# Performance work log

Measured on AMD Instinct MI355X. Metric: run time of the kernel, lower is better.

The kernel has to match this reference:

```python
import jax, jax.numpy as jnp
import numpy as np

N = 100000
E = 1600000
NEG_SLOPE = 0.2


def gat_conv(h_x, edge_index, W, a_src, a_dst, b, heads, concat):
    # h_x: [N, Fin]; W: [Fin, heads*C]
    n = h_x.shape[0]
    h = (h_x @ W).reshape(n, heads, -1)              # [N, H, C]
    s_src = (h * a_src[None]).sum(-1)                # [N, H]
    s_dst = (h * a_dst[None]).sum(-1)                # [N, H]
    # add self loops (PyG default)
    loop = jnp.arange(n, dtype=edge_index.dtype)
    src = jnp.concatenate([edge_index[0], loop])
    dst = jnp.concatenate([edge_index[1], loop])
    e = jax.nn.leaky_relu(s_src[src] + s_dst[dst], NEG_SLOPE)   # [E+N, H]
    m = jax.ops.segment_max(e, dst, num_segments=n)
    e = jnp.exp(e - m[dst])
    denom = jax.ops.segment_sum(e, dst, num_segments=n)
    alpha = e / denom[dst]                                       # [E+N, H]
    out = jax.ops.segment_sum(alpha[:, :, None] * h[src], dst, num_segments=n)  # [N,H,C]
    out = out.reshape(n, -1) if concat else out.mean(axis=1)
    return out + b


def setup_inputs() -> dict:
    key = jax.random.key(0)
    ks = jax.random.split(key, 16)
    s = 0.1
    return {
        "x": jax.random.normal(ks[0], (N, 128), jnp.float32),
        "edge_index": jax.random.randint(ks[1], (2, E), 0, N, jnp.int64 if jax.config.jax_enable_x64 else jnp.int32),
        "W0": jax.random.normal(ks[2], (128, 64), jnp.float32) * s,
        "a_src0": jax.random.normal(ks[3], (1, 64), jnp.float32) * s,
        "a_dst0": jax.random.normal(ks[4], (1, 64), jnp.float32) * s,
        "b0": jax.random.normal(ks[5], (64,), jnp.float32) * s,
        "sW0": jax.random.normal(ks[6], (128, 64), jnp.float32) * s,
        "sb0": jax.random.normal(ks[7], (64,), jnp.float32) * s,
        "W1": jax.random.normal(ks[8], (64, 32), jnp.float32) * s,
        "a_src1": jax.random.normal(ks[9], (1, 32), jnp.float32) * s,
        "a_dst1": jax.random.normal(ks[10], (1, 32), jnp.float32) * s,
        "b1": jax.random.normal(ks[11], (32,), jnp.float32) * s,
        "sW1": jax.random.normal(ks[12], (64, 32), jnp.float32) * s,
        "sb1": jax.random.normal(ks[13], (32,), jnp.float32) * s,
    }


def reference(x, edge_index, W0, a_src0, a_dst0, b0, sW0, sb0,
              W1, a_src1, a_dst1, b1, sW1, sb1):
    # layer 0: GATConv (heads=1, concat=True) + linear skip, ELU (dropout p=0 is identity)
    h = gat_conv(x, edge_index, W0, a_src0, a_dst0, b0, heads=1, concat=True) + (x @ sW0 + sb0)
    h = jax.nn.elu(h)
    # layer 1: GATConv (heads=1, concat=False -> mean) + linear skip, log_softmax
    h = gat_conv(h, edge_index, W1, a_src1, a_dst1, b1, heads=1, concat=False) + (h @ sW1 + sb1)
    return jax.nn.log_softmax(h, axis=-1)
```

## Files before the change

kernel.cpp:

```cpp
#include <hip/hip_runtime.h>
#include <hip/hip_bf16.h>
#include <math.h>

#define NEG_SLOPE 0.2f
#define ECLAMP 30.0f
#define HCLAMP 1.0e4f

#define BSHIFT 8
#define BR 256
#define NBMAX 1024
#define CHUNK 2048

typedef short v8s __attribute__((ext_vector_type(8)));
typedef float v4f __attribute__((ext_vector_type(4)));
typedef unsigned long long ull;

__device__ __forceinline__ float bf2f(__hip_bfloat16 v) { return __bfloat162float(v); }
__device__ __forceinline__ __hip_bfloat16 f2bf(float v) { return __float2bfloat16(v); }
__device__ __forceinline__ float sane(float v)   { return fminf(fmaxf(v, -HCLAMP), HCLAMP); }
__device__ __forceinline__ float eclampf(float v){ return fminf(fmaxf(v, -ECLAMP), ECLAMP); }

__device__ __forceinline__ float ldany(int isf32, const void* p, int i) {
    return isf32 ? ((const float*)p)[i] : bf2f(((const __hip_bfloat16*)p)[i]);
}
__device__ __forceinline__ int ldidx(int is64, const void* p, long long i) {
    return is64 ? (int)((const long long*)p)[i] : ((const int*)p)[i];
}
__device__ __forceinline__ v8s ld8(const __hip_bfloat16* p) { return *(const v8s*)p; }

__device__ __forceinline__ float ewgt(float e) {
    e = e > 0.f ? e : NEG_SLOPE * e;
    return __expf(eclampf(e));
}

__device__ __forceinline__ float bflo(unsigned v) { return __uint_as_float(v << 16); }
__device__ __forceinline__ float bfhi(unsigned v) { return __uint_as_float(v & 0xffff0000u); }
__device__ __forceinline__ unsigned packbf(float a, float b) {
    __hip_bfloat16 x = f2bf(a), y = f2bf(b);
    return (unsigned)(*(unsigned short*)&x) | ((unsigned)(*(unsigned short*)&y) << 16);
}

__global__ void k_probe(const unsigned* __restrict__ xw, int nw_safe,
                        const unsigned* __restrict__ ew, int* __restrict__ flags) {
    __shared__ int cnt[2];
    int t = threadIdx.x;
    if (t < 2) cnt[t] = 0;
    __syncthreads();
    unsigned w = xw[(unsigned)(t * 9973) % (unsigned)nw_safe];
    unsigned lo = w & 0xffffu;
    unsigned exp = (lo >> 7) & 0xffu;
    if (lo != 0u && (exp < 90u || exp > 160u)) atomicAdd(&cnt[0], 1);
    if (ew[2 * t + 1] == 0u) atomicAdd(&cnt[1], 1);
    __syncthreads();
    if (t == 0) { flags[0] = (2 * cnt[0] > 256) ? 1 : 0; flags[1] = (cnt[1] >= 200) ? 1 : 0; }
}

__global__ void k_params(const int* __restrict__ flags,
                         const void* W0, const void* sW0, const void* as0, const void* ad0,
                         const void* b0, const void* sb0, const void* W1, const void* sW1,
                         const void* as1, const void* ad1, const void* b1, const void* sb1,
                         float* __restrict__ Pf, __hip_bfloat16* __restrict__ Wg) {
    int f = flags[0];
    int t = blockIdx.x * blockDim.x + threadIdx.x;
    int T = gridDim.x * blockDim.x;
    for (int i = t; i < 8192; i += T) {
        int n = i >> 7, k = i & 127;
        Wg[i]        = f2bf(ldany(f, W0,  k * 64 + n));
        Wg[8192 + i] = f2bf(ldany(f, sW0, k * 64 + n));
    }
    for (int i = t; i < 2048; i += T) {
        int n = i >> 6, k = i & 63;
        Wg[16384 + i] = f2bf(ldany(f, W1,  k * 32 + n));
        Wg[18432 + i] = f2bf(ldany(f, sW1, k * 32 + n));
    }
    if (t < 64) {
        Pf[t]       = ldany(f, as0, t);
        Pf[64 + t]  = ldany(f, ad0, t);
        Pf[128 + t] = ldany(f, b0, t) + ldany(f, sb0, t);
    }
    if (t < 32) {
        Pf[192 + t] = ldany(f, as1, t);
        Pf[224 + t] = ldany(f, ad1, t);
        Pf[256 + t] = ldany(f, b1, t) + ldany(f, sb1, t);
    }
}

__global__ void k_zero(int* __restrict__ p, int n) {
    int i = blockIdx.x * blockDim.x + threadIdx.x;
    if (i < n) p[i] = 0;
}

__global__ __launch_bounds__(256) void k_bcount(const void* __restrict__ ei,
                                                const int* __restrict__ flags,
                                                int E, int N, int NB,
                                                int* __restrict__ bcount) {
    __shared__ int h[NBMAX];
    for (int i = threadIdx.x; i < NB; i += 256) h[i] = 0;
    __syncthreads();
    int f = flags[1];
    int stride = gridDim.x * 256;
    for (int i = blockIdx.x * 256 + threadIdx.x; i < E; i += stride) {
        unsigned d = (unsigned)ldidx(f, ei, (long long)E + i);
        if (d < (unsigned)N) atomicAdd(&h[d >> BSHIFT], 1);
    }
    __syncthreads();
    for (int i = threadIdx.x; i < NB; i += 256) {
        int c = h[i];
        if (c) atomicAdd(&bcount[i], c);
    }
}

__global__ void k_bscan(const int* __restrict__ bcount, int NB,
                        int* __restrict__ bbase, int* __restrict__ bcursor) {
    __shared__ int sh[NBMAX];
    int t = threadIdx.x;
    int v = (t < NB) ? bcount[t] : 0;
    sh[t] = v;
    __syncthreads();
    for (int off = 1; off < NBMAX; off <<= 1) {
        int xv = (t >= off) ? sh[t - off] : 0;
        __syncthreads();
        sh[t] += xv;
        __syncthreads();
    }
    if (t < NB) {
        int e = sh[t] - v;
        bbase[t] = e;
        bcursor[t] = e;
    }
    if (t == NB - 1) bbase[NB] = sh[t];
}

__global__ __launch_bounds__(256) void k_bscatter(const void* __restrict__ ei,
                                                  const int* __restrict__ flags,
                                                  int E, int N, int NB,
                                                  int* __restrict__ bcursor,
                                                  unsigned* __restrict__ binned) {
    __shared__ int h[NBMAX];
    __shared__ int rb[NBMAX];
    int f = flags[1];
    long long c0 = (long long)blockIdx.x * CHUNK;
    long long c1 = c0 + CHUNK;
    if (c1 > E) c1 = E;
    for (int i = threadIdx.x; i < NB; i += 256) h[i] = 0;
    __syncthreads();
    for (long long i = c0 + threadIdx.x; i < c1; i += 256) {
        unsigned d = (unsigned)ldidx(f, ei, (long long)E + i);
        if (d < (unsigned)N) atomicAdd(&h[d >> BSHIFT], 1);
    }
    __syncthreads();
    for (int i = threadIdx.x; i < NB; i += 256) {
        int c = h[i];
        rb[i] = c ? atomicAdd(&bcursor[i], c) : 0;
        h[i] = 0;
    }
    __syncthreads();
    for (long long i = c0 + threadIdx.x; i < c1; i += 256) {
        unsigned d = (unsigned)ldidx(f, ei, (long long)E + i);
        if (d < (unsigned)N) {
            int b = d >> BSHIFT;
            unsigned s = (unsigned)ldidx(f, ei, i);
            if (s >= (unsigned)N) s = 0x00FFFFFFu;
            int r = atomicAdd(&h[b], 1);
            binned[rb[b] + r] = ((d & (unsigned)(BR - 1)) << 24) | s;
        }
    }
}

__global__ __launch_bounds__(256) void k_bbuild(const unsigned* __restrict__ binned,
                                                const int* __restrict__ bbase,
                                                int N, int NB,
                                                int* __restrict__ rowptr,
                                                int* __restrict__ csr_src) {
    __shared__ int ldeg[BR];
    __shared__ int lpos[BR];
    int b = blockIdx.x;
    int t = threadIdx.x;
    int e0 = bbase[b], e1 = bbase[b + 1];
    ldeg[t] = 0;
    __syncthreads();
    for (int i = e0 + t; i < e1; i += 256) {
        atomicAdd(&ldeg[binned[i] >> 24], 1);
    }
    __syncthreads();
    int v = ldeg[t];
    lpos[t] = v;
    __syncthreads();
    for (int off = 1; off < BR; off <<= 1) {
        int xv = (t >= off) ? lpos[t - off] : 0;
        __syncthreads();
        lpos[t] += xv;
        __syncthreads();
    }
    int excl = lpos[t] - v;
    int node = (b << BSHIFT) + t;
    if (node < N) rowptr[node] = e0 + excl;
    if (b == NB - 1 && t == 0) rowptr[N] = e1;
    ldeg[t] = e0 + excl;
    __syncthreads();
    for (int i = e0 + t; i < e1; i += 256) {
        unsigned w = binned[i];
        int p = atomicAdd(&ldeg[w >> 24], 1);
        csr_src[p] = (int)(w & 0x00FFFFFFu);
    }
}

__global__ void k_deg(const void* __restrict__ ei, const int* __restrict__ flags,
                      int E, int N, int* __restrict__ deg) {
    int i = blockIdx.x * blockDim.x + threadIdx.x;
    if (i < E) {
        unsigned d = (unsigned)ldidx(flags[1], ei, (long long)E + i);
        if (d < (unsigned)N) atomicAdd(&deg[d], 1);
    }
}

__global__ void k_scan1(const int* __restrict__ deg, int N,
                        int* __restrict__ rowptr, int* __restrict__ bsum) {
    __shared__ int sh[1024];
    int t = threadIdx.x;
    int idx = blockIdx.x * 1024 + t;
    int v = (idx < N) ? deg[idx] : 0;
    sh[t] = v;
    __syncthreads();
    for (int off = 1; off < 1024; off <<= 1) {
        int xv = (t >= off) ? sh[t - off] : 0;
        __syncthreads();
        sh[t] += xv;
        __syncthreads();
    }
    if (idx < N) rowptr[idx] = sh[t] - v;
    if (t == 1023) bsum[blockIdx.x] = sh[1023];
}

__global__ void k_scan2(int* __restrict__ bsum, int B, int* __restrict__ rowptr, int N) {
    __shared__ int sh[1024];
    int t = threadIdx.x;
    int v = (t < B) ? bsum[t] : 0;
    sh[t] = v;
    __syncthreads();
    for (int off = 1; off < 1024; off <<= 1) {
        int xv = (t >= off) ? sh[t - off] : 0;
        __syncthreads();
        sh[t] += xv;
        __syncthreads();
    }
    if (t < B) bsum[t] = sh[t] - v;
    if (t == 1023) rowptr[N] = sh[1023];
}

__global__ void k_scan3(int N, int* __restrict__ rowptr, const int* __restrict__ bsum,
                        int* __restrict__ cursor) {
    int idx = blockIdx.x * 1024 + threadIdx.x;
    if (idx < N) {
        int r = rowptr[idx] + bsum[blockIdx.x];
        rowptr[idx] = r;
        cursor[idx] = r;
    }
}

__global__ void k_fill(const void* __restrict__ ei, const int* __restrict__ flags,
                       int E, int N, int* __restrict__ cursor, int* __restrict__ csr_src) {
    int i = blockIdx.x * blockDim.x + threadIdx.x;
    if (i < E) {
        int f = flags[1];
        unsigned d = (unsigned)ldidx(f, ei, (long long)E + i);
        if (d < (unsigned)N) {
            int p = atomicAdd(&cursor[d], 1);
            if ((unsigned)p < (unsigned)E) csr_src[p] = ldidx(f, ei, i);
        }
    }
}

__global__ __launch_bounds__(256) void k_l0(
    const void* __restrict__ x, const int* __restrict__ flags,
    const float* __restrict__ Pf, const __hip_bfloat16* __restrict__ Wg, int N,
    __hip_bfloat16* __restrict__ h0, __hip_bfloat16* __restrict__ skip0,
    float* __restrict__ ssrc, float* __restrict__ sdst) {
    __shared__ __hip_bfloat16 sm[26112];
    __hip_bfloat16* xs  = sm;
    __hip_bfloat16* wt0 = sm + 8704;
    __hip_bfloat16* wts = sm + 17408;
    int tid = threadIdx.x;
    int f = flags[0];
    int tile = blockIdx.x * 64;

    for (int i = tid * 4; i < 8192; i += 1024) {
        int r = i >> 7, k = i & 127;
        __hip_bfloat16* d0 = &wt0[r * 136 + k];
        __hip_bfloat16* d1 = &wts[r * 136 + k];
#pragma unroll
        for (int u = 0; u < 4; u++) { d0[u] = Wg[i + u]; d1[u] = Wg[8192 + i + u]; }
    }
    for (int i = tid * 4; i < 8192; i += 1024) {
        int r = i >> 7, k = i & 127;
        int g = tile + r; if (g >= N) g = N - 1;
        __hip_bfloat16* dx = &xs[r * 136 + k];
        if (f) {
            const float* xp = (const float*)x + (size_t)g * 128 + k;
#pragma unroll
            for (int u = 0; u < 4; u++) dx[u] = f2bf(xp[u]);
        } else {
            const __hip_bfloat16* xp = (const __hip_bfloat16*)x + (size_t)g * 128 + k;
#pragma unroll
            for (int u = 0; u < 4; u++) dx[u] = xp[u];
        }
    }
    __syncthreads();

    int lane = tid & 63, w = tid >> 6;
    int n16 = lane & 15, quad = lane >> 4;
    v4f zf = {0.f, 0.f, 0.f, 0.f};
    v4f acc_h[4], acc_s[4];
#pragma unroll
    for (int t = 0; t < 4; t++) { acc_h[t] = zf; acc_s[t] = zf; }

    int arow = (w << 4) + n16;
#pragma unroll
    for (int s = 0; s < 4; s++) {
        v8s a = ld8(&xs[arow * 136 + s * 32 + (quad << 3)]);
#pragma unroll
        for (int t = 0; t < 4; t++) {
            v8s bh = ld8(&wt0[(t * 16 + n16) * 136 + s * 32 + (quad << 3)]);
            acc_h[t] = __builtin_amdgcn_mfma_f32_16x16x32_bf16(a, bh, acc_h[t], 0, 0, 0);
            v8s bs = ld8(&wts[(t * 16 + n16) * 136 + s * 32 + (quad << 3)]);
            acc_s[t] = __builtin_amdgcn_mfma_f32_16x16x32_bf16(a, bs, acc_s[t], 0, 0, 0);
        }
    }

    int mbase = tile + (w << 4) + (quad << 2);
    float ps[4] = {0, 0, 0, 0}, pd[4] = {0, 0, 0, 0};
#pragma unroll
    for (int t = 0; t < 4; t++) {
        int ch = t * 16 + n16;
        float av = Pf[ch];
        float dv = Pf[64 + ch];
        float bv = Pf[128 + ch];
#pragma unroll
        for (int r = 0; r < 4; r++) {
            float hv = sane(acc_h[t][r]);
            float sv = sane(acc_s[t][r] + bv);
            int node = mbase + r;
            if (node < N) {
                h0[(size_t)node * 64 + ch] = f2bf(hv);
                skip0[(size_t)node * 64 + ch] = f2bf(sv);
            }
            ps[r] += hv * av;
            pd[r] += hv * dv;
        }
    }
#pragma unroll
    for (int m = 1; m <= 8; m <<= 1) {
#pragma unroll
        for (int r = 0; r < 4; r++) {
            ps[r] += __shfl_xor(ps[r], m, 64);
            pd[r] += __shfl_xor(pd[r], m, 64);
        }
    }
    if (n16 == 0) {
#pragma unroll
        for (int r = 0; r < 4; r++) {
            int node = mbase + r;
            if (node < N) { ssrc[node] = sane(ps[r]); sdst[node] = sane(pd[r]); }
        }
    }
}

__global__ __launch_bounds__(256) void k_l0_agg(
    const int* __restrict__ rowptr, const int* __restrict__ csr_src,
    const float* __restrict__ ssrc, const float* __restrict__ sdst,
    const __hip_bfloat16* __restrict__ h0,
    int N, __hip_bfloat16* __restrict__ skip0_hact) {
    __shared__ ull ews[256];
    int wv = threadIdx.x >> 6, lane = threadIdx.x & 63;
    int half = lane >> 5, l5 = lane & 31;
    int slot = l5 >> 4, c4 = l5 & 15;
    int n = blockIdx.x * 8 + wv * 2 + half;
    bool act = n < N;
    int nn = act ? n : 0;
    const uint2* h0w = (const uint2*)h0;
    ull* myw = &ews[wv * 64 + half * 32];

    float sd = sdst[nn];
    float wself = ewgt(ssrc[nn] + sd);

    uint2 selfv = h0w[(size_t)nn * 16 + c4];
    float w0 = (slot == 0) ? wself : 0.f;
    float acc0 = w0 * bflo(selfv.x);
    float acc1 = w0 * bfhi(selfv.x);
    float acc2 = w0 * bflo(selfv.y);
    float acc3 = w0 * bfhi(selfv.y);
    float denp = 0.f;

    int beg = act ? rowptr[nn] : 0;
    int end = act ? rowptr[nn + 1] : 0;
    for (int j0 = beg; j0 < end; j0 += 32) {
        int cnt = end - j0; if (cnt > 32) cnt = 32;
        int s = (l5 < cnt) ? csr_src[j0 + l5] : 0;
        bool v = (l5 < cnt) && ((unsigned)s < (unsigned)N);
        int sg = v ? s : 0;
        float wj = v ? ewgt(ssrc[sg] + sd) : 0.f;
        denp += wj;
        myw[l5] = ((ull)__float_as_uint(wj) << 32) | (unsigned)sg;
        for (int k2 = 0; k2 < cnt; k2 += 4) {
            int ia = k2 + slot, ib = k2 + 2 + slot;
            ull pa = myw[ia < cnt ? ia : 0];
            ull pb = myw[ib < cnt ? ib : 0];
            float wa = (ia < cnt) ? __uint_as_float((unsigned)(pa >> 32)) : 0.f;
            float wb = (ib < cnt) ? __uint_as_float((unsigned)(pb >> 32)) : 0.f;
            int sa = (int)(unsigned)(pa & 0xffffffffu);
            int sb = (int)(unsigned)(pb & 0xffffffffu);
            uint2 va = h0w[(size_t)sa * 16 + c4];
            uint2 vb = h0w[(size_t)sb * 16 + c4];
            acc0 += wa * bflo(va.x) + wb * bflo(vb.x);
            acc1 += wa * bfhi(va.x) + wb * bfhi(vb.x);
            acc2 += wa * bflo(va.y) + wb * bflo(vb.y);
            acc3 += wa * bfhi(va.y) + wb * bfhi(vb.y);
        }
    }
    acc0 += __shfl_xor(acc0, 16, 64);
    acc1 += __shfl_xor(acc1, 16, 64);
    acc2 += __shfl_xor(acc2, 16, 64);
    acc3 += __shfl_xor(acc3, 16, 64);
    float den = denp;
#pragma unroll
    for (int m = 1; m <= 16; m <<= 1) den += __shfl_xor(den, m, 64);
    den += wself;

    if (slot == 0 && act) {
        uint2 skv = ((const uint2*)skip0_hact)[(size_t)nn * 16 + c4];
        float v0 = sane(acc0 / den + bflo(skv.x));
        float v1 = sane(acc1 / den + bfhi(skv.x));
        float v2 = sane(acc2 / den + bflo(skv.y));
        float v3 = sane(acc3 / den + bfhi(skv.y));
        v0 = v0 > 0.f ? v0 : (__expf(v0) - 1.f);
        v1 = v1 > 0.f ? v1 : (__expf(v1) - 1.f);
        v2 = v2 > 0.f ? v2 : (__expf(v2) - 1.f);
        v3 = v3 > 0.f ? v3 : (__expf(v3) - 1.f);
        uint2 o;
        o.x = packbf(v0, v1);
        o.y = packbf(v2, v3);
        ((uint2*)skip0_hact)[(size_t)nn * 16 + c4] = o;
    }
}

__global__ __launch_bounds__(256) void k_l1(
    const __hip_bfloat16* __restrict__ hact,
    const float* __restrict__ Pf, const __hip_bfloat16* __restrict__ Wg, int N,
    __hip_bfloat16* __restrict__ h1, __hip_bfloat16* __restrict__ skip1,
    float* __restrict__ ssrc, float* __restrict__ sdst) {
    __shared__ __hip_bfloat16 sm[9216];
    __hip_bfloat16* xs  = sm;
    __hip_bfloat16* wt1 = sm + 4608;
    __hip_bfloat16* ws1 = sm + 6912;
    int tid = threadIdx.x;
    int tile = blockIdx.x * 64;

    for (int i = tid * 4; i < 2048; i += 1024) {
        int r = i >> 6, k = i & 63;
        __hip_bfloat16* d0 = &wt1[r * 72 + k];
        __hip_bfloat16* d1 = &ws1[r * 72 + k];
#pragma unroll
        for (int u = 0; u < 4; u++) { d0[u] = Wg[16384 + i + u]; d1[u] = Wg[18432 + i + u]; }
    }
    for (int i = tid * 4; i < 4096; i += 1024) {
        int r = i >> 6, k = i & 63;
        int g = tile + r; if (g >= N) g = N - 1;
        __hip_bfloat16* dx = &xs[r * 72 + k];
        const __hip_bfloat16* xp = hact + (size_t)g * 64 + k;
#pragma unroll
        for (int u = 0; u < 4; u++) dx[u] = xp[u];
    }
    __syncthreads();

    int lane = tid & 63, w = tid >> 6;
    int n16 = lane & 15, quad = lane >> 4;
    v4f zf = {0.f, 0.f, 0.f, 0.f};
    v4f acc_h[2], acc_s[2];
#pragma unroll
    for (int t = 0; t < 2; t++) { acc_h[t] = zf; acc_s[t] = zf; }

    int arow = (w << 4) + n16;
#pragma unroll
    for (int s = 0; s < 2; s++) {
        v8s a = ld8(&xs[arow * 72 + s * 32 + (quad << 3)]);
#pragma unroll
        for (int t = 0; t < 2; t++) {
            v8s bh = ld8(&wt1[(t * 16 + n16) * 72 + s * 32 + (quad << 3)]);
            acc_h[t] = __builtin_amdgcn_mfma_f32_16x16x32_bf16(a, bh, acc_h[t], 0, 0, 0);
            v8s bs = ld8(&ws1[(t * 16 + n16) * 72 + s * 32 + (quad << 3)]);
            acc_s[t] = __builtin_amdgcn_mfma_f32_16x16x32_bf16(a, bs, acc_s[t], 0, 0, 0);
        }
    }

    int mbase = tile + (w << 4) + (quad << 2);
    float ps[4] = {0, 0, 0, 0}, pd[4] = {0, 0, 0, 0};
#pragma unroll
    for (int t = 0; t < 2; t++) {
        int ch = t * 16 + n16;
        float av = Pf[192 + ch];
        float dv = Pf[224 + ch];
        float bv = Pf[256 + ch];
#pragma unroll
        for (int r = 0; r < 4; r++) {
            float hv = sane(acc_h[t][r]);
            float sv = sane(acc_s[t][r] + bv);
            int node = mbase + r;
            if (node < N) {
                h1[(size_t)node * 32 + ch] = f2bf(hv);
                skip1[(size_t)node * 32 + ch] = f2bf(sv);
            }
            ps[r] += hv * av;
            pd[r] += hv * dv;
        }
    }
#pragma unroll
    for (int m = 1; m <= 8; m <<= 1) {
#pragma unroll
        for (int r = 0; r < 4; r++) {
            ps[r] += __shfl_xor(ps[r], m, 64);
            pd[r] += __shfl_xor(pd[r], m, 64);
        }
    }
    if (n16 == 0) {
#pragma unroll
        for (int r = 0; r < 4; r++) {
            int node = mbase + r;
            if (node < N) { ssrc[node] = sane(ps[r]); sdst[node] = sane(pd[r]); }
        }
    }
}

__global__ __launch_bounds__(256) void k_l1_agg(
    const int* __restrict__ rowptr, const int* __restrict__ csr_src,
    const float* __restrict__ ssrc, const float* __restrict__ sdst,
    const __hip_bfloat16* __restrict__ h1, const __hip_bfloat16* __restrict__ skip1,
    int N, float* __restrict__ out) {
    __shared__ ull ews[256];
    int wv = threadIdx.x >> 6, lane = threadIdx.x & 63;
    int half = lane >> 5, l5 = lane & 31;
    int slot = l5 >> 3, c4 = l5 & 7;
    int n = blockIdx.x * 8 + wv * 2 + half;
    bool act = n < N;
    int nn = act ? n : 0;
    const uint2* h1w = (const uint2*)h1;
    ull* myw = &ews[wv * 64 + half * 32];

    float sd = sdst[nn];
    float wself = ewgt(ssrc[nn] + sd);

    uint2 selfv = h1w[(size_t)nn * 8 + c4];
    float w0 = (slot == 0) ? wself : 0.f;
    float acc0 = w0 * bflo(selfv.x);
    float acc1 = w0 * bfhi(selfv.x);
    float acc2 = w0 * bflo(selfv.y);
    float acc3 = w0 * bfhi(selfv.y);
    float denp = 0.f;

    int beg = act ? rowptr[nn] : 0;
    int end = act ? rowptr[nn + 1] : 0;
    for (int j0 = beg; j0 < end; j0 += 32) {
        int cnt = end - j0; if (cnt > 32) cnt = 32;
        int s = (l5 < cnt) ? csr_src[j0 + l5] : 0;
        bool v = (l5 < cnt) && ((unsigned)s < (unsigned)N);
        int sg = v ? s : 0;
        float wj = v ? ewgt(ssrc[sg] + sd) : 0.f;
        denp += wj;
        myw[l5] = ((ull)__float_as_uint(wj) << 32) | (unsigned)sg;
        for (int k4 = 0; k4 < cnt; k4 += 8) {
            int ia = k4 + slot, ib = k4 + 4 + slot;
            ull pa = myw[ia < cnt ? ia : 0];
            ull pb = myw[ib < cnt ? ib : 0];
            float wa = (ia < cnt) ? __uint_as_float((unsigned)(pa >> 32)) : 0.f;
            float wb = (ib < cnt) ? __uint_as_float((unsigned)(pb >> 32)) : 0.f;
            int sa = (int)(unsigned)(pa & 0xffffffffu);
            int sb = (int)(unsigned)(pb & 0xffffffffu);
            uint2 va = h1w[(size_t)sa * 8 + c4];
            uint2 vb = h1w[(size_t)sb * 8 + c4];
            acc0 += wa * bflo(va.x) + wb * bflo(vb.x);
            acc1 += wa * bfhi(va.x) + wb * bfhi(vb.x);
            acc2 += wa * bflo(va.y) + wb * bflo(vb.y);
            acc3 += wa * bfhi(va.y) + wb * bfhi(vb.y);
        }
    }
    acc0 += __shfl_xor(acc0, 8, 64); acc0 += __shfl_xor(acc0, 16, 64);
    acc1 += __shfl_xor(acc1, 8, 64); acc1 += __shfl_xor(acc1, 16, 64);
    acc2 += __shfl_xor(acc2, 8, 64); acc2 += __shfl_xor(acc2, 16, 64);
    acc3 += __shfl_xor(acc3, 8, 64); acc3 += __shfl_xor(acc3, 16, 64);
    float den = denp;
#pragma unroll
    for (int m = 1; m <= 16; m <<= 1) den += __shfl_xor(den, m, 64);
    den += wself;

    uint2 skv = ((const uint2*)skip1)[(size_t)nn * 8 + c4];
    float o0 = sane(acc0 / den + bflo(skv.x));
    float o1 = sane(acc1 / den + bfhi(skv.x));
    float o2 = sane(acc2 / den + bflo(skv.y));
    float o3 = sane(acc3 / den + bfhi(skv.y));
    float m = fmaxf(fmaxf(o0, o1), fmaxf(o2, o3));
#pragma unroll
    for (int k = 1; k <= 4; k <<= 1) m = fmaxf(m, __shfl_xor(m, k, 64));
    float ex = __expf(o0 - m) + __expf(o1 - m) + __expf(o2 - m) + __expf(o3 - m);
#pragma unroll
    for (int k = 1; k <= 4; k <<= 1) ex += __shfl_xor(ex, k, 64);
    float l = __logf(ex);
    float r0 = o0 - m - l, r1 = o1 - m - l, r2 = o2 - m - l, r3 = o3 - m - l;
    if (!isfinite(r0)) r0 = 0.f;
    if (!isfinite(r1)) r1 = 0.f;
    if (!isfinite(r2)) r2 = 0.f;
    if (!isfinite(r3)) r3 = 0.f;
    if (slot == 0 && act) {
        float4 o4; o4.x = r0; o4.y = r1; o4.z = r2; o4.w = r3;
        *(float4*)&out[(size_t)nn * 32 + 4 * c4] = o4;
    }
}

__global__ void k_sentinel(float* __restrict__ out, int n, float val) {
    int i = blockIdx.x * blockDim.x + threadIdx.x;
    if (i < n) out[i] = val;
}

extern "C" void kernel_launch(void* const* d_in, const int* in_sizes, int n_in,
                              void* d_out, int out_size, void* d_ws, size_t ws_size,
                              hipStream_t stream) {
    const void* x  = d_in[0];
    const void* ei = d_in[1];
    float* out = (float*)d_out;

    int N = in_sizes[0] / 128;
    int E = in_sizes[1] / 2;

    char* ws = (char*)d_ws;
    size_t off = 0;
    auto alloc = [&](size_t bytes) -> char* {
        char* p = ws + off;
        off += (bytes + 255) & ~(size_t)255;
        return p;
    };
    int*   flags   = (int*)alloc(2 * 4);
    float* Pf      = (float*)alloc(288 * 4);
    __hip_bfloat16* Wg = (__hip_bfloat16*)alloc(20480 * 2);
    int*   rowptr  = (int*)alloc((size_t)(N + 1) * 4);
    int*   cursor  = (int*)alloc((size_t)N * 4);
    float* sdst01  = (float*)alloc((size_t)N * 4);
    int*   bsum    = (int*)alloc(1024 * 4);
    int*   bcount  = (int*)alloc(NBMAX * 4);
    int*   bbase   = (int*)alloc((NBMAX + 1) * 4);
    int*   bcursor = (int*)alloc(NBMAX * 4);
    int*   csr_src = (int*)alloc((size_t)E * 4);
    __hip_bfloat16* h0    = (__hip_bfloat16*)alloc((size_t)N * 64 * 2);
    __hip_bfloat16* skip0 = (__hip_bfloat16*)alloc((size_t)N * 64 * 2);
    size_t required = off;

    if (ws_size < required) {
        float mb = (float)(double)(ws_size >> 20);
        k_sentinel<<<(out_size + 255) / 256, 256, 0, stream>>>(out, out_size, mb);
        return;
    }

    float* ssrc01 = (float*)cursor;
    __hip_bfloat16* h1    = h0;
    __hip_bfloat16* skip1 = h0 + (size_t)N * 32;

    k_probe<<<1, 256, 0, stream>>>((const unsigned*)x, N * 64, (const unsigned*)ei, flags);
    k_params<<<40, 256, 0, stream>>>(flags, d_in[2], d_in[6], d_in[3], d_in[4],
                                     d_in[5], d_in[7], d_in[8], d_in[12],
                                     d_in[9], d_in[10], d_in[11], d_in[13], Pf, Wg);

    int NB = (N + BR - 1) >> BSHIFT;
    bool fast = (N <= (NBMAX << BSHIFT)) && ((size_t)E * 4 <= (size_t)N * 128);

    if (fast) {
        unsigned* binned = (unsigned*)h0;
        int gch = (E + CHUNK - 1) / CHUNK;
        if (gch < 1) gch = 1;
        int gcount = (E + 255) / 256;
        if (gcount > 1024) gcount = 1024;
        k_zero<<<(NB + 255) / 256, 256, 0, stream>>>(bcount, NB);
        k_bcount<<<gcount, 256, 0, stream>>>(ei, flags, E, N, NB, bcount);
        k_bscan<<<1, NBMAX, 0, stream>>>(bcount, NB, bbase, bcursor);
        k_bscatter<<<gch, 256, 0, stream>>>(ei, flags, E, N, NB, bcursor, binned);
        k_bbuild<<<NB, 256, 0, stream>>>(binned, bbase, N, NB, rowptr, csr_src);
    } else {
        int B = (N + 1023) / 1024;
        k_zero<<<(N + 255) / 256, 256, 0, stream>>>(cursor, N);
        k_deg<<<(E + 255) / 256, 256, 0, stream>>>(ei, flags, E, N, cursor);
        k_scan1<<<B, 1024, 0, stream>>>(cursor, N, rowptr, bsum);
        k_scan2<<<1, 1024, 0, stream>>>(bsum, B, rowptr, N);
        k_scan3<<<B, 1024, 0, stream>>>(N, rowptr, bsum, cursor);
        k_fill<<<(E + 255) / 256, 256, 0, stream>>>(ei, flags, E, N, cursor, csr_src);
    }

    k_l0<<<(N + 63) / 64, 256, 0, stream>>>(x, flags, Pf, Wg, N,
                                            h0, skip0, ssrc01, sdst01);
    k_l0_agg<<<(N + 7) / 8, 256, 0, stream>>>(rowptr, csr_src, ssrc01, sdst01,
                                              h0, N, skip0);
    k_l1<<<(N + 63) / 64, 256, 0, stream>>>(skip0, Pf, Wg, N,
                                            h1, skip1, ssrc01, sdst01);
    k_l1_agg<<<(N + 7) / 8, 256, 0, stream>>>(rowptr, csr_src, ssrc01, sdst01,
                                              h1, skip1, N, out);
}
```

Before: 301.0 us.

## Replace atomic bucket cursors with per-chunk histogram scan; unroll aggregation loops

The bucket sort now writes a per-chunk histogram, scans it per bucket to get deterministic chunk offsets, and the scatter kernel no longer recounts edges or uses global atomics on bucket cursors. This removes the second pass over destination indices in the scatter kernel and the global atomic contention. In exchange it adds a histogram buffer (chunks x buckets) plus a scan kernel that reads it column-strided. Separately, both aggregation inner loops are unrolled to issue four gathers per step instead of two, which should raise memory-level parallelism at some cost in registers.

```diff
diff --git a/kernel.cpp b/kernel.cpp
--- a/kernel.cpp
+++ b/kernel.cpp
@@ -90,28 +90,54 @@
     if (i < n) p[i] = 0;
 }
 
-__global__ __launch_bounds__(256) void k_bcount(const void* __restrict__ ei,
-                                                const int* __restrict__ flags,
-                                                int E, int N, int NB,
-                                                int* __restrict__ bcount) {
+__global__ __launch_bounds__(256) void k_chist(const void* __restrict__ ei,
+                                               const int* __restrict__ flags,
+                                               int E, int N, int NB,
+                                               int* __restrict__ hist) {
     __shared__ int h[NBMAX];
     for (int i = threadIdx.x; i < NB; i += 256) h[i] = 0;
     __syncthreads();
     int f = flags[1];
-    int stride = gridDim.x * 256;
-    for (int i = blockIdx.x * 256 + threadIdx.x; i < E; i += stride) {
+    long long c0 = (long long)blockIdx.x * CHUNK;
+    long long c1 = c0 + CHUNK;
+    if (c1 > E) c1 = E;
+    for (long long i = c0 + threadIdx.x; i < c1; i += 256) {
         unsigned d = (unsigned)ldidx(f, ei, (long long)E + i);
         if (d < (unsigned)N) atomicAdd(&h[d >> BSHIFT], 1);
     }
     __syncthreads();
-    for (int i = threadIdx.x; i < NB; i += 256) {
-        int c = h[i];
-        if (c) atomicAdd(&bcount[i], c);
-    }
+    long long base = (long long)blockIdx.x * NB;
+    for (int i = threadIdx.x; i < NB; i += 256) hist[base + i] = h[i];
+}
+
+__global__ __launch_bounds__(1024) void k_cscan(const int* __restrict__ hist,
+                                                int gch, int NB,
+                                                int* __restrict__ cb,
+                                                int* __restrict__ bcount) {
+    __shared__ int sh[1024];
+    int b = blockIdx.x;
+    int t = threadIdx.x;
+    int run = 0;
+    for (int base = 0; base < gch; base += 1024) {
+        int c = base + t;
+        int v = (c < gch) ? hist[(long long)c * NB + b] : 0;
+        sh[t] = v;
+        __syncthreads();
+        for (int off = 1; off < 1024; off <<= 1) {
+            int xv = (t >= off) ? sh[t - off] : 0;
+            __syncthreads();
+            sh[t] += xv;
+            __syncthreads();
+        }
+        if (c < gch) cb[(long long)c * NB + b] = run + sh[t] - v;
+        run += sh[1023];
+        __syncthreads();
+    }
+    if (t == 0) bcount[b] = run;
 }
 
 __global__ void k_bscan(const int* __restrict__ bcount, int NB,
-                        int* __restrict__ bbase, int* __restrict__ bcursor) {
+                        int* __restrict__ bbase) {
     __shared__ int sh[NBMAX];
     int t = threadIdx.x;
     int v = (t < NB) ? bcount[t] : 0;
@@ -123,46 +149,32 @@
         sh[t] += xv;
         __syncthreads();
     }
-    if (t < NB) {
-        int e = sh[t] - v;
-        bbase[t] = e;
-        bcursor[t] = e;
-    }
+    if (t < NB) bbase[t] = sh[t] - v;
     if (t == NB - 1) bbase[NB] = sh[t];
 }
 
 __global__ __launch_bounds__(256) void k_bscatter(const void* __restrict__ ei,
                                                   const int* __restrict__ flags,
                                                   int E, int N, int NB,
-                                                  int* __restrict__ bcursor,
+                                                  const int* __restrict__ bbase,
+                                                  const int* __restrict__ cb,
                                                   unsigned* __restrict__ binned) {
-    __shared__ int h[NBMAX];
     __shared__ int rb[NBMAX];
     int f = flags[1];
+    long long cbase = (long long)blockIdx.x * NB;
+    for (int i = threadIdx.x; i < NB; i += 256) rb[i] = bbase[i] + cb[cbase + i];
+    __syncthreads();
     long long c0 = (long long)blockIdx.x * CHUNK;
     long long c1 = c0 + CHUNK;
     if (c1 > E) c1 = E;
-    for (int i = threadIdx.x; i < NB; i += 256) h[i] = 0;
-    __syncthreads();
-    for (long long i = c0 + threadIdx.x; i < c1; i += 256) {
-        unsigned d = (unsigned)ldidx(f, ei, (long long)E + i);
-        if (d < (unsigned)N) atomicAdd(&h[d >> BSHIFT], 1);
-    }
-    __syncthreads();
-    for (int i = threadIdx.x; i < NB; i += 256) {
-        int c = h[i];
-        rb[i] = c ? atomicAdd(&bcursor[i], c) : 0;
-        h[i] = 0;
-    }
-    __syncthreads();
     for (long long i = c0 + threadIdx.x; i < c1; i += 256) {
         unsigned d = (unsigned)ldidx(f, ei, (long long)E + i);
         if (d < (unsigned)N) {
             int b = d >> BSHIFT;
             unsigned s = (unsigned)ldidx(f, ei, i);
             if (s >= (unsigned)N) s = 0x00FFFFFFu;
-            int r = atomicAdd(&h[b], 1);
-            binned[rb[b] + r] = ((d & (unsigned)(BR - 1)) << 24) | s;
+            int r = atomicAdd(&rb[b], 1);
+            binned[r] = ((d & (unsigned)(BR - 1)) << 24) | s;
         }
     }
 }
@@ -401,20 +413,29 @@
         float wj = v ? ewgt(ssrc[sg] + sd) : 0.f;
         denp += wj;
         myw[l5] = ((ull)__float_as_uint(wj) << 32) | (unsigned)sg;
-        for (int k2 = 0; k2 < cnt; k2 += 4) {
-            int ia = k2 + slot, ib = k2 + 2 + slot;
+        for (int k2 = 0; k2 < cnt; k2 += 8) {
+            int ia = k2 + slot,     ib = k2 + 2 + slot;
+            int ic = k2 + 4 + slot, id = k2 + 6 + slot;
             ull pa = myw[ia < cnt ? ia : 0];
             ull pb = myw[ib < cnt ? ib : 0];
+            ull pc = myw[ic < cnt ? ic : 0];
+            ull pd_ = myw[id < cnt ? id : 0];
             float wa = (ia < cnt) ? __uint_as_float((unsigned)(pa >> 32)) : 0.f;
             float wb = (ib < cnt) ? __uint_as_float((unsigned)(pb >> 32)) : 0.f;
+            float wc = (ic < cnt) ? __uint_as_float((unsigned)(pc >> 32)) : 0.f;
+            float wd = (id < cnt) ? __uint_as_float((unsigned)(pd_ >> 32)) : 0.f;
             int sa = (int)(unsigned)(pa & 0xffffffffu);
             int sb = (int)(unsigned)(pb & 0xffffffffu);
+            int sc = (int)(unsigned)(pc & 0xffffffffu);
+            int sdi = (int)(unsigned)(pd_ & 0xffffffffu);
             uint2 va = h0w[(size_t)sa * 16 + c4];
             uint2 vb = h0w[(size_t)sb * 16 + c4];
-            acc0 += wa * bflo(va.x) + wb * bflo(vb.x);
-            acc1 += wa * bfhi(va.x) + wb * bfhi(vb.x);
-            acc2 += wa * bflo(va.y) + wb * bflo(vb.y);
-            acc3 += wa * bfhi(va.y) + wb * bfhi(vb.y);
+            uint2 vc = h0w[(size_t)sc * 16 + c4];
+            uint2 vd = h0w[(size_t)sdi * 16 + c4];
+            acc0 += wa * bflo(va.x) + wb * bflo(vb.x) + wc * bflo(vc.x) + wd * bflo(vd.x);
+            acc1 += wa * bfhi(va.x) + wb * bfhi(vb.x) + wc * bfhi(vc.x) + wd * bfhi(vd.x);
+            acc2 += wa * bflo(va.y) + wb * bflo(vb.y) + wc * bflo(vc.y) + wd * bflo(vd.y);
+            acc3 += wa * bfhi(va.y) + wb * bfhi(vb.y) + wc * bfhi(vc.y) + wd * bfhi(vd.y);
         }
     }
     acc0 += __shfl_xor(acc0, 16, 64);
@@ -566,20 +587,29 @@
         float wj = v ? ewgt(ssrc[sg] + sd) : 0.f;
         denp += wj;
         myw[l5] = ((ull)__float_as_uint(wj) << 32) | (unsigned)sg;
-        for (int k4 = 0; k4 < cnt; k4 += 8) {
-            int ia = k4 + slot, ib = k4 + 4 + slot;
+        for (int k4 = 0; k4 < cnt; k4 += 16) {
+            int ia = k4 + slot,      ib = k4 + 4 + slot;
+            int ic = k4 + 8 + slot,  id = k4 + 12 + slot;
             ull pa = myw[ia < cnt ? ia : 0];
             ull pb = myw[ib < cnt ? ib : 0];
+            ull pc = myw[ic < cnt ? ic : 0];
+            ull pd_ = myw[id < cnt ? id : 0];
             float wa = (ia < cnt) ? __uint_as_float((unsigned)(pa >> 32)) : 0.f;
             float wb = (ib < cnt) ? __uint_as_float((unsigned)(pb >> 32)) : 0.f;
+            float wc = (ic < cnt) ? __uint_as_float((unsigned)(pc >> 32)) : 0.f;
+            float wd = (id < cnt) ? __uint_as_float((unsigned)(pd_ >> 32)) : 0.f;
             int sa = (int)(unsigned)(pa & 0xffffffffu);
             int sb = (int)(unsigned)(pb & 0xffffffffu);
+            int sc = (int)(unsigned)(pc & 0xffffffffu);
+            int sdi = (int)(unsigned)(pd_ & 0xffffffffu);
             uint2 va = h1w[(size_t)sa * 8 + c4];
             uint2 vb = h1w[(size_t)sb * 8 + c4];
-            acc0 += wa * bflo(va.x) + wb * bflo(vb.x);
-            acc1 += wa * bfhi(va.x) + wb * bfhi(vb.x);
-            acc2 += wa * bflo(va.y) + wb * bflo(vb.y);
-            acc3 += wa * bfhi(va.y) + wb * bfhi(vb.y);
+            uint2 vc = h1w[(size_t)sc * 8 + c4];
+            uint2 vd = h1w[(size_t)sdi * 8 + c4];
+            acc0 += wa * bflo(va.x) + wb * bflo(vb.x) + wc * bflo(vc.x) + wd * bflo(vd.x);
+            acc1 += wa * bfhi(va.x) + wb * bfhi(vb.x) + wc * bfhi(vc.x) + wd * bfhi(vd.x);
+            acc2 += wa * bflo(va.y) + wb * bflo(vb.y) + wc * bflo(vc.y) + wd * bflo(vd.y);
+            acc3 += wa * bfhi(va.y) + wb * bfhi(vb.y) + wc * bfhi(vc.y) + wd * bfhi(vd.y);
         }
     }
     acc0 += __shfl_xor(acc0, 8, 64); acc0 += __shfl_xor(acc0, 16, 64);
@@ -628,6 +658,11 @@
 
     int N = in_sizes[0] / 128;
     int E = in_sizes[1] / 2;
+
+    int NB  = (N + BR - 1) >> BSHIFT;
+    int gch = (E + CHUNK - 1) / CHUNK;
+    if (gch < 1) gch = 1;
+    bool fast = (N <= (NBMAX << BSHIFT)) && ((size_t)E * 4 <= (size_t)N * 128);
 
     char* ws = (char*)d_ws;
     size_t off = 0;
@@ -645,8 +680,9 @@
     int*   bsum    = (int*)alloc(1024 * 4);
     int*   bcount  = (int*)alloc(NBMAX * 4);
     int*   bbase   = (int*)alloc((NBMAX + 1) * 4);
-    int*   bcursor = (int*)alloc(NBMAX * 4);
     int*   csr_src = (int*)alloc((size_t)E * 4);
+    int*   hist    = (int*)alloc(fast ? (size_t)gch * NB * 4 : 0);
+    int*   cb      = (int*)alloc(fast ? (size_t)gch * NB * 4 : 0);
     __hip_bfloat16* h0    = (__hip_bfloat16*)alloc((size_t)N * 64 * 2);
     __hip_bfloat16* skip0 = (__hip_bfloat16*)alloc((size_t)N * 64 * 2);
     size_t required = off;
@@ -666,19 +702,12 @@
                                      d_in[5], d_in[7], d_in[8], d_in[12],
                                      d_in[9], d_in[10], d_in[11], d_in[13], Pf, Wg);
 
-    int NB = (N + BR - 1) >> BSHIFT;
-    bool fast = (N <= (NBMAX << BSHIFT)) && ((size_t)E * 4 <= (size_t)N * 128);
-
     if (fast) {
         unsigned* binned = (unsigned*)h0;
-        int gch = (E + CHUNK - 1) / CHUNK;
-        if (gch < 1) gch = 1;
-        int gcount = (E + 255) / 256;
-        if (gcount > 1024) gcount = 1024;
-        k_zero<<<(NB + 255) / 256, 256, 0, stream>>>(bcount, NB);
-        k_bcount<<<gcount, 256, 0, stream>>>(ei, flags, E, N, NB, bcount);
-        k_bscan<<<1, NBMAX, 0, stream>>>(bcount, NB, bbase, bcursor);
-        k_bscatter<<<gch, 256, 0, stream>>>(ei, flags, E, N, NB, bcursor, binned);
+        k_chist<<<gch, 256, 0, stream>>>(ei, flags, E, N, NB, hist);
+        k_cscan<<<NB, 1024, 0, stream>>>(hist, gch, NB, cb, bcount);
+        k_bscan<<<1, NBMAX, 0, stream>>>(bcount, NB, bbase);
+        k_bscatter<<<gch, 256, 0, stream>>>(ei, flags, E, N, NB, bbase, cb, binned);
         k_bbuild<<<NB, 256, 0, stream>>>(binned, bbase, N, NB, rowptr, csr_src);
     } else {
         int B = (N + 1023) / 1024;
```

New measurement: 269.6 us. 10.5% less time.
